# Kernel tuning notes

Measured on AMD Instinct MI355X. Metric: run time of the kernel, lower is better.

The kernel has to match this reference:

```python
import jax, jax.numpy as jnp
import numpy as np

K = 5          # kernel_size
BETA = 15.0    # soft-max temperature
PAD = (K - 1) // 2  # fixed_padding with dilation=1: pad_beg = pad_end = 2


def setup_inputs() -> dict:
    key = jax.random.key(0)
    kx, kw = jax.random.split(key)
    x = jax.random.normal(kx, (16, 8, 256, 256), dtype=jnp.float32)
    weight = jax.random.normal(kw, (8, 8, K, K), dtype=jnp.float32) * 0.1
    return {"x": x, "weight": weight}


def reference(x, weight):
    """Morphological dilation2d with soft-max (logsumexp) reduction.

    Equivalent to: unfold(pad(x)) -> (B,1,C*K*K,L); add weight.view(O,-1);
    logsumexp(beta * .) / beta over the C*K*K axis; reshape to (B,O,H,W).
    Implemented as a streaming logsumexp over the K*K taps to avoid the
    huge unfold intermediate.
    """
    B, C, H, W = x.shape
    O = weight.shape[0]
    xp = jnp.pad(x, ((0, 0), (0, 0), (PAD, PAD), (PAD, PAD)))
    acc = None
    for ki in range(K):
        for kj in range(K):
            xs = xp[:, :, ki:ki + H, kj:kj + W]              # (B,C,H,W)
            w_tap = weight[:, :, ki, kj]                      # (O,C)
            # beta * (w + x), broadcast to (B,O,C,H,W)
            t = BETA * (xs[:, None, :, :, :] + w_tap[None, :, :, None, None])
            lse = jax.nn.logsumexp(t, axis=2)                 # (B,O,H,W)
            acc = lse if acc is None else jnp.logaddexp(acc, lse)
    return acc / BETA
```

## Files before the change

kernel.cpp:

```cpp
#include <hip/hip_runtime.h>
#include <math.h>

#define KW 5
#define BETA 15.0f
#define MSHIFT 3.0f
#define CIN 8
#define COUT 8
#define HH 256
#define WW 256
#define TW 64
#define THT 16
#define CWp 68
#define CHp 20

typedef float f32x4 __attribute__((ext_vector_type(4)));
typedef short s16x8 __attribute__((ext_vector_type(8)));

static __device__ __forceinline__ short f2bf(float f) {
    unsigned u = __float_as_uint(f);
    unsigned r = (u + 0x7FFFu + ((u >> 16) & 1u)) >> 16;
    return (short)r;
}

__global__ __launch_bounds__(256, 4) void morph_mfma(
    const float* __restrict__ x, const float* __restrict__ wgt,
    float* __restrict__ out)
{
    __shared__ int4 exs[CHp * CWp];

    const int tid  = threadIdx.x;
    const int lane = tid & 63;
    const int wv   = tid >> 6;
    const int px   = lane & 15;
    const int quad = lane >> 4;

    const int lid = blockIdx.x;
    const int sw  = (lid & 7) * 128 + (lid >> 3);
    const int b   = sw >> 6;
    const int t   = sw & 63;
    const int h0  = (t >> 2) * THT;
    const int w0  = (t & 3) * TW;

    s16x8 afrag[7];
    int   toff[7];
    #pragma unroll
    for (int g = 0; g < 7; ++g) {
        int tap = g * 4 + quad;
        int tc  = tap < 25 ? tap : 24;
        toff[g] = (tc / KW) * CWp + (tc % KW);
        s16x8 af;
        #pragma unroll
        for (int j = 0; j < 8; ++j) {
            float v = 0.0f;
            if (tap < 25 && px < COUT)
                v = __expf(BETA * wgt[(px * CIN + j) * (KW * KW) + tap]);
            af[j] = f2bf(v);
        }
        afrag[g] = af;
    }

    for (int s = tid; s < CHp * CWp; s += 256) {
        int r = s / CWp, col = s - r * CWp;
        int gh = h0 + r - 2, gw = w0 + col - 2;
        bool ok = ((unsigned)gh < (unsigned)HH) & ((unsigned)gw < (unsigned)WW);
        unsigned pk[4];
        #pragma unroll
        for (int c2 = 0; c2 < 4; ++c2) {
            float v0 = 0.0f, v1 = 0.0f;
            if (ok) {
                v0 = x[((b * CIN + 2 * c2) * HH + gh) * WW + gw];
                v1 = x[((b * CIN + 2 * c2 + 1) * HH + gh) * WW + gw];
            }
            unsigned lo = (unsigned short)f2bf(__expf(BETA * (v0 - MSHIFT)));
            unsigned hi = (unsigned short)f2bf(__expf(BETA * (v1 - MSHIFT)));
            pk[c2] = lo | (hi << 16);
        }
        int4 p; p.x = pk[0]; p.y = pk[1]; p.z = pk[2]; p.w = pk[3];
        exs[s] = p;
    }
    __syncthreads();

    const float inv_beta = 1.0f / BETA;
    for (int wb = 0; wb < 4; ++wb) {
        #pragma unroll
        for (int hl = 0; hl < 4; ++hl) {
            const int hh   = wv * 4 + hl;
            const int base = hh * CWp + wb * 16 + px;
            f32x4 acc = {0.0f, 0.0f, 0.0f, 0.0f};
            #pragma unroll
            for (int g = 0; g < 7; ++g) {
                s16x8 bfr = *(const s16x8*)&exs[base + toff[g]];
                acc = __builtin_amdgcn_mfma_f32_16x16x32_bf16(
                          afrag[g], bfr, acc, 0, 0, 0);
            }
            if (quad < 2) {
                #pragma unroll
                for (int r = 0; r < 4; ++r) {
                    int o = quad * 4 + r;
                    out[((b * COUT + o) * HH + h0 + hh) * WW + w0 + wb * 16 + px]
                        = MSHIFT + __logf(acc[r]) * inv_beta;
                }
            }
        }
    }
}

extern "C" void kernel_launch(void* const* d_in, const int* in_sizes, int n_in,
                              void* d_out, int out_size, void* d_ws, size_t ws_size,
                              hipStream_t stream) {
    const float* x   = (const float*)d_in[0];
    const float* wgt = (const float*)d_in[1];
    float* out = (float*)d_out;

    const int B = in_sizes[0] / (CIN * HH * WW);
    const int nblk = B * (HH / THT) * (WW / TW);
    morph_mfma<<<nblk, 256, 0, stream>>>(x, wgt, out);
}
```

Measured before the change: 111.1 us.

## Shrink tile width, vectorize halo loads, split MFMA accumulators

Tile width drops from 64 to 32 columns, so each block stages a smaller halo and twice as many blocks launch, with the launch-bounds occupancy hint raised to 8. The shared-memory fill now reads four consecutive columns per channel with a float4 load and falls back to scalar loads only at image borders. The MFMA chain is split into two independent accumulators to shorten the dependency chain, and the output loop is fully unrolled. The narrower tile raises halo overhead per output pixel, and the occupancy hint may force register spilling.

Result: slower. 139.8 us (+25.8%).

```diff
diff --git a/kernel.cpp b/kernel.cpp
--- a/kernel.cpp
+++ b/kernel.cpp
@@ -8,21 +8,20 @@
 #define COUT 8
 #define HH 256
 #define WW 256
-#define TW 64
+#define TW 32
 #define THT 16
-#define CWp 68
+#define CWp 36
 #define CHp 20
 
 typedef float f32x4 __attribute__((ext_vector_type(4)));
 typedef short s16x8 __attribute__((ext_vector_type(8)));
 
-static __device__ __forceinline__ short f2bf(float f) {
+static __device__ __forceinline__ unsigned f2bf(float f) {
     unsigned u = __float_as_uint(f);
-    unsigned r = (u + 0x7FFFu + ((u >> 16) & 1u)) >> 16;
-    return (short)r;
+    return (u + 0x7FFFu + ((u >> 16) & 1u)) >> 16;
 }
 
-__global__ __launch_bounds__(256, 4) void morph_mfma(
+__global__ __launch_bounds__(256, 8) void morph_mfma(
     const float* __restrict__ x, const float* __restrict__ wgt,
     float* __restrict__ out)
 {
@@ -35,11 +34,11 @@
     const int quad = lane >> 4;
 
     const int lid = blockIdx.x;
-    const int sw  = (lid & 7) * 128 + (lid >> 3);
-    const int b   = sw >> 6;
-    const int t   = sw & 63;
-    const int h0  = (t >> 2) * THT;
-    const int w0  = (t & 3) * TW;
+    const int sw  = (lid & 7) * 256 + (lid >> 3);
+    const int b   = sw >> 7;
+    const int t   = sw & 127;
+    const int h0  = (t >> 3) * THT;
+    const int w0  = (t & 7) * TW;
 
     s16x8 afrag[7];
     int   toff[7];
@@ -54,51 +53,73 @@
             float v = 0.0f;
             if (tap < 25 && px < COUT)
                 v = __expf(BETA * wgt[(px * CIN + j) * (KW * KW) + tap]);
-            af[j] = f2bf(v);
+            af[j] = (short)f2bf(v);
         }
         afrag[g] = af;
     }
 
-    for (int s = tid; s < CHp * CWp; s += 256) {
-        int r = s / CWp, col = s - r * CWp;
-        int gh = h0 + r - 2, gw = w0 + col - 2;
-        bool ok = ((unsigned)gh < (unsigned)HH) & ((unsigned)gw < (unsigned)WW);
-        unsigned pk[4];
+    for (int s = tid; s < CHp * (CWp / 4); s += 256) {
+        int r  = s / (CWp / 4);
+        int q  = s - r * (CWp / 4);
+        int gh = h0 + r - 2;
+        int gw0 = w0 + 4 * q - 2;
+        bool rowok = (unsigned)gh < (unsigned)HH;
+        bool fast  = rowok & (gw0 >= 0) & (gw0 + 3 < WW);
+        unsigned pk[4][4];
         #pragma unroll
-        for (int c2 = 0; c2 < 4; ++c2) {
-            float v0 = 0.0f, v1 = 0.0f;
-            if (ok) {
-                v0 = x[((b * CIN + 2 * c2) * HH + gh) * WW + gw];
-                v1 = x[((b * CIN + 2 * c2 + 1) * HH + gh) * WW + gw];
+        for (int c = 0; c < CIN; ++c) {
+            float v[4];
+            if (fast) {
+                const float4 f = *(const float4*)&x[((b * CIN + c) * HH + gh) * WW + gw0];
+                v[0] = f.x; v[1] = f.y; v[2] = f.z; v[3] = f.w;
+            } else {
+                #pragma unroll
+                for (int e = 0; e < 4; ++e) {
+                    int gw = gw0 + e;
+                    v[e] = (rowok && (unsigned)gw < (unsigned)WW)
+                         ? x[((b * CIN + c) * HH + gh) * WW + gw] : 0.0f;
+                }
             }
-            unsigned lo = (unsigned short)f2bf(__expf(BETA * (v0 - MSHIFT)));
-            unsigned hi = (unsigned short)f2bf(__expf(BETA * (v1 - MSHIFT)));
-            pk[c2] = lo | (hi << 16);
+            #pragma unroll
+            for (int e = 0; e < 4; ++e) {
+                unsigned bfv = f2bf(__expf(BETA * (v[e] - MSHIFT)));
+                if (c & 1) pk[e][c >> 1] |= bfv << 16;
+                else       pk[e][c >> 1]  = bfv;
+            }
         }
-        int4 p; p.x = pk[0]; p.y = pk[1]; p.z = pk[2]; p.w = pk[3];
-        exs[s] = p;
+        #pragma unroll
+        for (int e = 0; e < 4; ++e) {
+            int4 p; p.x = pk[e][0]; p.y = pk[e][1]; p.z = pk[e][2]; p.w = pk[e][3];
+            exs[r * CWp + 4 * q + e] = p;
+        }
     }
     __syncthreads();
 
     const float inv_beta = 1.0f / BETA;
-    for (int wb = 0; wb < 4; ++wb) {
+    #pragma unroll
+    for (int wb = 0; wb < 2; ++wb) {
         #pragma unroll
         for (int hl = 0; hl < 4; ++hl) {
             const int hh   = wv * 4 + hl;
             const int base = hh * CWp + wb * 16 + px;
-            f32x4 acc = {0.0f, 0.0f, 0.0f, 0.0f};
+            f32x4 acc0 = {0.0f, 0.0f, 0.0f, 0.0f};
+            f32x4 acc1 = {0.0f, 0.0f, 0.0f, 0.0f};
             #pragma unroll
             for (int g = 0; g < 7; ++g) {
                 s16x8 bfr = *(const s16x8*)&exs[base + toff[g]];
-                acc = __builtin_amdgcn_mfma_f32_16x16x32_bf16(
-                          afrag[g], bfr, acc, 0, 0, 0);
+                if (g & 1)
+                    acc1 = __builtin_amdgcn_mfma_f32_16x16x32_bf16(
+                               afrag[g], bfr, acc1, 0, 0, 0);
+                else
+                    acc0 = __builtin_amdgcn_mfma_f32_16x16x32_bf16(
+                               afrag[g], bfr, acc0, 0, 0, 0);
             }
             if (quad < 2) {
                 #pragma unroll
                 for (int r = 0; r < 4; ++r) {
                     int o = quad * 4 + r;
                     out[((b * COUT + o) * HH + h0 + hh) * WW + w0 + wb * 16 + px]
-                        = MSHIFT + __logf(acc[r]) * inv_beta;
+                        = MSHIFT + __logf(acc0[r] + acc1[r]) * inv_beta;
                 }
             }
         }
```
